# Optimization experiments

Measured on AMD Instinct MI355X. Metric: run time of the kernel, lower is better.

Reference implementation:

```python
import jax, jax.numpy as jnp
import numpy as np
from jax import lax

C = 64      # mid_channels
CR = 16     # reduced channels (C // reduction_ratio 4)
G = 4       # groups (C // group_channels 16)
K = 7       # involution kernel size
L = 6       # number of involution layers (n_layers - 2)
EPS = 1e-5
DN = ('NCHW', 'OIHW', 'NCHW')


def conv3(x, w, b):
    # 3x3 conv, stride 1, no padding (torch Conv2d default)
    y = lax.conv_general_dilated(x, w, (1, 1), [(0, 0), (0, 0)], dimension_numbers=DN)
    return y + b[None, :, None, None]


def conv1x1(x, w, b):
    # pointwise conv as einsum over channels
    return jnp.einsum('oi,bihw->bohw', w, x) + b[None, :, None, None]


def involution(x, wr, br, g, bt, mu, var, ws, bs):
    B, Cc, H, W = x.shape
    # kernel generation: 1x1 reduce -> BN (eval) -> ReLU -> 1x1 span
    t = conv1x1(x, wr, br)
    t = (t - mu[None, :, None, None]) * (g * jax.lax.rsqrt(var + EPS))[None, :, None, None] + bt[None, :, None, None]
    t = jax.nn.relu(t)
    w = conv1x1(t, ws, bs)                    # (B, G*K*K, H, W)
    w = w.reshape(B, G, K * K, H, W)
    # unfold: patches ordered (C, Kh, Kw) along channel dim, matching torch unfold
    p = lax.conv_general_dilated_patches(x, (K, K), (1, 1), [(K // 2, K // 2)] * 2, dimension_numbers=DN)
    p = p.reshape(B, G, Cc // G, K * K, H, W)
    out = jnp.einsum('bgkhw,bgckhw->bgchw', w, p)
    return out.reshape(B, Cc, H, W)


def setup_inputs() -> dict:
    key = jax.random.key(0)
    ks = jax.random.split(key, 9)
    s = 0.05
    return {
        'input_tensor': jax.random.normal(ks[0], (1, 3, 128, 128), jnp.float32),
        'conv_in_w': jax.random.normal(ks[1], (C, 3, 3, 3), jnp.float32) * s,
        'conv_in_b': jax.random.normal(ks[2], (C,), jnp.float32) * s,
        'w_reduce': jax.random.normal(ks[3], (L, CR, C), jnp.float32) * s,
        'b_reduce': jax.random.normal(ks[4], (L, CR), jnp.float32) * s,
        'bn_gamma': jnp.ones((L, CR), jnp.float32),
        'bn_beta': jnp.zeros((L, CR), jnp.float32),
        'bn_mean': jnp.zeros((L, CR), jnp.float32),
        'bn_var': jnp.ones((L, CR), jnp.float32),
        'w_span': jax.random.normal(ks[5], (L, G * K * K, CR), jnp.float32) * s,
        'b_span': jax.random.normal(ks[6], (L, G * K * K), jnp.float32) * s,
        'conv_out_w': jax.random.normal(ks[7], (2 * C, C, 3, 3), jnp.float32) * s,
        'conv_out_b': jax.random.normal(ks[8], (2 * C,), jnp.float32) * s,
    }


def reference(input_tensor, conv_in_w, conv_in_b, w_reduce, b_reduce, bn_gamma,
              bn_beta, bn_mean, bn_var, w_span, b_span, conv_out_w, conv_out_b):
    x = conv3(input_tensor, conv_in_w, conv_in_b)          # (1, 64, 126, 126)
    for i in range(L):
        x = jax.nn.relu(involution(x, w_reduce[i], b_reduce[i], bn_gamma[i],
                                   bn_beta[i], bn_mean[i], bn_var[i],
                                   w_span[i], b_span[i]))
    return conv3(x, conv_out_w, conv_out_b)                # (1, 128, 124, 124)
```

## Files before the change

### kernel.cpp

```cpp
#include <hip/hip_runtime.h>

#define IH 126
#define IW 126
#define HW 15876
#define OH 124
#define OW 124
#define OHW 15376

__global__ __launch_bounds__(256) void conv_in_kernel(
    const float* __restrict__ x, const float* __restrict__ w,
    const float* __restrict__ b, float* __restrict__ y)
{
  int pix = blockIdx.x * 256 + threadIdx.x;
  if (pix >= HW) return;
  int oc = blockIdx.y;
  int h  = pix / IW;
  int wc = pix - h * IW;
  const float* wp = w + oc * 27;
  float acc = b[oc];
#pragma unroll
  for (int ci = 0; ci < 3; ci++)
#pragma unroll
    for (int ky = 0; ky < 3; ky++)
#pragma unroll
      for (int kx = 0; kx < 3; kx++)
        acc = fmaf(x[ci * 128 * 128 + (h + ky) * 128 + (wc + kx)],
                   wp[ci * 9 + ky * 3 + kx], acc);
  y[oc * HW + pix] = acc;
}

__global__ __launch_bounds__(512, 4) void inv_kernel(
    const float* __restrict__ x, float* __restrict__ y,
    const float* __restrict__ wr, const float* __restrict__ br,
    const float* __restrict__ gam, const float* __restrict__ bet,
    const float* __restrict__ mu, const float* __restrict__ var,
    const float* __restrict__ wspan, const float* __restrict__ bspan)
{
  __shared__ __align__(16) char smem[63664];
  float* xs  = (float*)smem;
  float* wvs = (float*)(smem + 36400);
  float* tss = (float*)(smem + 61488);
  float* ob  = (float*)smem;

  int tid = threadIdx.x;
  int bx = blockIdx.x & 15, by = blockIdx.x >> 4;
  int ox0 = bx * 8, oy0 = by * 4;
  int xh0 = ox0 - 3, yh0 = oy0 - 3;

  for (int idx = tid; idx < 140 * 64; idx += 512) {
    int c = idx / 140;
    int pos = idx - c * 140;
    int row = pos / 14;
    int col = pos - row * 14;
    int gy = yh0 + row, gx = xh0 + col;
    float v = 0.f;
    if (gy >= 0 && gy < IH && gx >= 0 && gx < IW)
      v = x[c * HW + gy * IW + gx];
    xs[pos * 65 + c] = v;
  }
  __syncthreads();

  int w  = __builtin_amdgcn_readfirstlane(tid >> 6);
  int ln = tid & 63;
  int p  = ln & 31;
  int s  = ln >> 5;

  {
    int cr = 2 * w + s;
    int prow = p >> 3, pcol = p & 7;
    int pos = (prow + 3) * 14 + (pcol + 3);
    const float* xr = &xs[pos * 65];
    const float* wrr = wr + cr * 64;
    float a = 0.f;
#pragma unroll
    for (int c = 0; c < 64; c++) a = fmaf(xr[c], wrr[c], a);
    float sc = gam[cr] * rsqrtf(var[cr] + 1e-5f);
    float t = (a + br[cr] - mu[cr]) * sc + bet[cr];
    tss[p * 17 + cr] = fmaxf(t, 0.f);
  }
  __syncthreads();

  {
    int g  = w & 3;
    int q2 = (w >> 2) * 2 + s;
    float t16[16];
#pragma unroll
    for (int i = 0; i < 16; i++) t16[i] = tss[p * 17 + i];
    int prow = p >> 3, pcol = p & 7;
    const float* wsb = wspan + g * 49 * 16;
    const float* bsb = bspan + g * 49;
    for (int k = q2; k < 49; k += 4) {
      const float* wk = wsb + k * 16;
      float a = bsb[k];
#pragma unroll
      for (int i = 0; i < 16; i++) a = fmaf(t16[i], wk[i], a);
      wvs[((g * 49 + k) * 8 + pcol) * 4 + prow] = a;
    }
  }
  __syncthreads();

  float acc0 = 0.f, acc1 = 0.f, acc2 = 0.f, acc3 = 0.f;
  {
    int c = ln;
    int g = c >> 4;
    float xw[4][7];
#pragma unroll
    for (int r = 0; r < 4; r++)
#pragma unroll
      for (int kx = 0; kx < 7; kx++)
        xw[r][kx] = xs[(r * 14 + w + kx) * 65 + c];
#pragma unroll
    for (int ky = 0; ky < 7; ky++) {
      if (ky > 0) {
#pragma unroll
        for (int r = 0; r < 3; r++)
#pragma unroll
          for (int kx = 0; kx < 7; kx++) xw[r][kx] = xw[r + 1][kx];
#pragma unroll
        for (int kx = 0; kx < 7; kx++)
          xw[3][kx] = xs[((ky + 3) * 14 + w + kx) * 65 + c];
      }
#pragma unroll
      for (int kx = 0; kx < 7; kx++) {
        int k = ky * 7 + kx;
        float4 w4 = *(const float4*)&wvs[((g * 49 + k) * 8 + w) * 4];
        acc0 = fmaf(w4.x, xw[0][kx], acc0);
        acc1 = fmaf(w4.y, xw[1][kx], acc1);
        acc2 = fmaf(w4.z, xw[2][kx], acc2);
        acc3 = fmaf(w4.w, xw[3][kx], acc3);
      }
    }
  }
  __syncthreads();

  {
    int c = ln;
    ob[c * 33 + 0 * 8 + w] = fmaxf(acc0, 0.f);
    ob[c * 33 + 1 * 8 + w] = fmaxf(acc1, 0.f);
    ob[c * 33 + 2 * 8 + w] = fmaxf(acc2, 0.f);
    ob[c * 33 + 3 * 8 + w] = fmaxf(acc3, 0.f);
  }
  __syncthreads();
  for (int j = tid; j < 2048; j += 512) {
    int c = j >> 5, pp = j & 31;
    int prow = pp >> 3, pcol = pp & 7;
    int gy = oy0 + prow, gx = ox0 + pcol;
    if (gy < IH && gx < IW)
      y[c * HW + gy * IW + gx] = ob[c * 33 + pp];
  }
}

__global__ __launch_bounds__(256) void transpose_w_kernel(
    const float* __restrict__ w, float* __restrict__ wt)
{
  int i = blockIdx.x * 256 + threadIdx.x;
  if (i >= 128 * 64 * 9) return;
  int oc = i / 576;
  int rem = i - oc * 576;
  int ci = rem / 9;
  int k = rem - ci * 9;
  wt[(k * 64 + ci) * 128 + oc] = w[i];
}

__global__ __launch_bounds__(512, 4) void conv_out_kernel(
    const float* __restrict__ x, const float* __restrict__ wt,
    const float* __restrict__ b, float* __restrict__ y)
{
  __shared__ __align__(16) float xsm[16 * 100 * 4];
  int tid = threadIdx.x;
  int bx = blockIdx.x & 15, by = blockIdx.x >> 4;
  int oy0 = by * 8, ox0 = bx * 8;

  for (int u = tid; u < 1600; u += 512) {
    int cq = u / 100;
    int pos = u - cq * 100;
    int row = pos / 10;
    int col = pos - row * 10;
    int gy = oy0 + row, gx = ox0 + col;
    float4 v = make_float4(0.f, 0.f, 0.f, 0.f);
    if (gy < IH && gx < IW) {
      const float* xp = x + cq * 4 * HW + gy * IW + gx;
      v.x = xp[0]; v.y = xp[HW]; v.z = xp[2 * HW]; v.w = xp[3 * HW];
    }
    *(float4*)&xsm[u * 4] = v;
  }
  __syncthreads();

  int ln = tid & 63;
  int px = ln & 7, py = ln >> 3;
  int wv_ = __builtin_amdgcn_readfirstlane(tid >> 6);
  int oc8 = blockIdx.y * 64 + wv_ * 8;

  float acc[8];
#pragma unroll
  for (int j = 0; j < 8; j++) acc[j] = b[oc8 + j];

#pragma unroll
  for (int ky = 0; ky < 3; ky++) {
#pragma unroll
    for (int kx = 0; kx < 3; kx++) {
      int k = ky * 3 + kx;
      int pidx = (py + ky) * 10 + px + kx;
      const float* wp = wt + k * 64 * 128 + oc8;
#pragma unroll 4
      for (int cq = 0; cq < 16; cq++) {
        float4 xv = *(const float4*)&xsm[(cq * 100 + pidx) * 4];
        const float* wq = wp + cq * 4 * 128;
#pragma unroll
        for (int j = 0; j < 8; j++) {
          acc[j] = fmaf(xv.x, wq[0 * 128 + j], acc[j]);
          acc[j] = fmaf(xv.y, wq[1 * 128 + j], acc[j]);
          acc[j] = fmaf(xv.z, wq[2 * 128 + j], acc[j]);
          acc[j] = fmaf(xv.w, wq[3 * 128 + j], acc[j]);
        }
      }
    }
  }

  int oy = oy0 + py, ox = ox0 + px;
  if (oy < OH && ox < OW) {
#pragma unroll
    for (int j = 0; j < 8; j++)
      y[(oc8 + j) * OHW + oy * OW + ox] = acc[j];
  }
}

extern "C" void kernel_launch(void* const* d_in, const int* in_sizes, int n_in,
                              void* d_out, int out_size, void* d_ws, size_t ws_size,
                              hipStream_t stream)
{
  const float* input = (const float*)d_in[0];
  const float* ciw   = (const float*)d_in[1];
  const float* cib   = (const float*)d_in[2];
  const float* wred  = (const float*)d_in[3];
  const float* bred  = (const float*)d_in[4];
  const float* gam   = (const float*)d_in[5];
  const float* bet   = (const float*)d_in[6];
  const float* mu    = (const float*)d_in[7];
  const float* var   = (const float*)d_in[8];
  const float* wspan = (const float*)d_in[9];
  const float* bspan = (const float*)d_in[10];
  const float* cow   = (const float*)d_in[11];
  const float* cob   = (const float*)d_in[12];
  float* out = (float*)d_out;

  float* bufA = (float*)d_ws;
  float* bufB = bufA + (1 << 20);
  float* wt   = bufA + (1 << 21);

  transpose_w_kernel<<<288, 256, 0, stream>>>(cow, wt);
  conv_in_kernel<<<dim3(63, 64), 256, 0, stream>>>(input, ciw, cib, bufA);

  float* cur = bufA; float* nxt = bufB;
  for (int i = 0; i < 6; i++) {
    inv_kernel<<<512, 512, 0, stream>>>(cur, nxt,
        wred + i * 16 * 64, bred + i * 16, gam + i * 16, bet + i * 16,
        mu + i * 16, var + i * 16, wspan + i * 196 * 16, bspan + i * 196);
    float* t = cur; cur = nxt; nxt = t;
  }
  conv_out_kernel<<<dim3(256, 2), 512, 0, stream>>>(cur, wt, cob, out);
}
```

Baseline: 254.6 us.

## Vectorize involution kernel-gen LDS reads and split conv_out into smaller blocks

Pads the shared x tile to 68 floats per position so the 1x1 reduce can read channels as float4, and has each wave compute two reduced channels for all 64 lanes. The span step is redistributed so each wave handles every eighth (group,k) pair, and a 20-float padded stride for the reduced activations allows float4 loads. conv_out moves to 256-thread blocks covering 32 output channels across four grid rows, which gives more blocks and better occupancy. The costs are redundant compute in half-idle lanes, an extra barrier, and the x tile being loaded twice as often in conv_out.

Measured after the change: 253.2 us. Within noise of the previous version (-0.5%).

```diff
diff --git a/kernel.cpp b/kernel.cpp
--- a/kernel.cpp
+++ b/kernel.cpp
@@ -36,11 +36,10 @@
     const float* __restrict__ mu, const float* __restrict__ var,
     const float* __restrict__ wspan, const float* __restrict__ bspan)
 {
-  __shared__ __align__(16) char smem[63664];
-  float* xs  = (float*)smem;
-  float* wvs = (float*)(smem + 36400);
-  float* tss = (float*)(smem + 61488);
-  float* ob  = (float*)smem;
+  __shared__ __align__(16) float xs[140][68];
+  __shared__ __align__(16) float wvs[6272];
+  float* tss = &wvs[5632];
+  float* ob  = &xs[0][0];
 
   int tid = threadIdx.x;
   int bx = blockIdx.x & 15, by = blockIdx.x >> 4;
@@ -56,45 +55,58 @@
     float v = 0.f;
     if (gy >= 0 && gy < IH && gx >= 0 && gx < IW)
       v = x[c * HW + gy * IW + gx];
-    xs[pos * 65 + c] = v;
-  }
-  __syncthreads();
-
-  int w  = __builtin_amdgcn_readfirstlane(tid >> 6);
+    xs[pos][c] = v;
+  }
+  __syncthreads();
+
+  int w_ = __builtin_amdgcn_readfirstlane(tid >> 6);
   int ln = tid & 63;
   int p  = ln & 31;
-  int s  = ln >> 5;
-
-  {
-    int cr = 2 * w + s;
-    int prow = p >> 3, pcol = p & 7;
-    int pos = (prow + 3) * 14 + (pcol + 3);
-    const float* xr = &xs[pos * 65];
-    const float* wrr = wr + cr * 64;
-    float a = 0.f;
-#pragma unroll
-    for (int c = 0; c < 64; c++) a = fmaf(xr[c], wrr[c], a);
-    float sc = gam[cr] * rsqrtf(var[cr] + 1e-5f);
-    float t = (a + br[cr] - mu[cr]) * sc + bet[cr];
-    tss[p * 17 + cr] = fmaxf(t, 0.f);
-  }
-  __syncthreads();
-
-  {
-    int g  = w & 3;
-    int q2 = (w >> 2) * 2 + s;
-    float t16[16];
-#pragma unroll
-    for (int i = 0; i < 16; i++) t16[i] = tss[p * 17 + i];
-    int prow = p >> 3, pcol = p & 7;
-    const float* wsb = wspan + g * 49 * 16;
-    const float* bsb = bspan + g * 49;
-    for (int k = q2; k < 49; k += 4) {
-      const float* wk = wsb + k * 16;
-      float a = bsb[k];
-#pragma unroll
-      for (int i = 0; i < 16; i++) a = fmaf(t16[i], wk[i], a);
-      wvs[((g * 49 + k) * 8 + pcol) * 4 + prow] = a;
+  int prow = p >> 3, pcol = p & 7;
+  int pc = (prow + 3) * 14 + (pcol + 3);
+
+  {
+    int cr0 = 2 * w_;
+    const float* wa = wr + cr0 * 64;
+    const float* wb = wa + 64;
+    float a0 = 0.f, a1 = 0.f;
+#pragma unroll
+    for (int ci = 0; ci < 64; ci += 4) {
+      float4 xv = *(const float4*)&xs[pc][ci];
+      a0 = fmaf(xv.x, wa[ci + 0], a0); a1 = fmaf(xv.x, wb[ci + 0], a1);
+      a0 = fmaf(xv.y, wa[ci + 1], a0); a1 = fmaf(xv.y, wb[ci + 1], a1);
+      a0 = fmaf(xv.z, wa[ci + 2], a0); a1 = fmaf(xv.z, wb[ci + 2], a1);
+      a0 = fmaf(xv.w, wa[ci + 3], a0); a1 = fmaf(xv.w, wb[ci + 3], a1);
+    }
+    float s0 = gam[cr0]     * rsqrtf(var[cr0]     + 1e-5f);
+    float s1 = gam[cr0 + 1] * rsqrtf(var[cr0 + 1] + 1e-5f);
+    float t0 = (a0 + br[cr0]     - mu[cr0])     * s0 + bet[cr0];
+    float t1 = (a1 + br[cr0 + 1] - mu[cr0 + 1]) * s1 + bet[cr0 + 1];
+    if (ln < 32) {
+      tss[p * 20 + cr0]     = fmaxf(t0, 0.f);
+      tss[p * 20 + cr0 + 1] = fmaxf(t1, 0.f);
+    }
+  }
+  __syncthreads();
+
+  {
+    float tv[16];
+#pragma unroll
+    for (int i = 0; i < 4; i++) {
+      float4 t4 = *(const float4*)&tss[p * 20 + 4 * i];
+      tv[4 * i] = t4.x; tv[4 * i + 1] = t4.y;
+      tv[4 * i + 2] = t4.z; tv[4 * i + 3] = t4.w;
+    }
+    __syncthreads();
+    for (int j = 0; j < 25; j++) {
+      int pair = w_ + 8 * j;
+      if (pair < 196) {
+        const float* wk = wspan + pair * 16;
+        float a = bspan[pair];
+#pragma unroll
+        for (int i = 0; i < 16; i++) a = fmaf(tv[i], wk[i], a);
+        if (ln < 32) wvs[pair * 32 + pcol * 4 + prow] = a;
+      }
     }
   }
   __syncthreads();
@@ -102,13 +114,13 @@
   float acc0 = 0.f, acc1 = 0.f, acc2 = 0.f, acc3 = 0.f;
   {
     int c = ln;
-    int g = c >> 4;
+    int g = ln >> 4;
     float xw[4][7];
 #pragma unroll
     for (int r = 0; r < 4; r++)
 #pragma unroll
       for (int kx = 0; kx < 7; kx++)
-        xw[r][kx] = xs[(r * 14 + w + kx) * 65 + c];
+        xw[r][kx] = xs[r * 14 + w_ + kx][c];
 #pragma unroll
     for (int ky = 0; ky < 7; ky++) {
       if (ky > 0) {
@@ -118,12 +130,12 @@
           for (int kx = 0; kx < 7; kx++) xw[r][kx] = xw[r + 1][kx];
 #pragma unroll
         for (int kx = 0; kx < 7; kx++)
-          xw[3][kx] = xs[((ky + 3) * 14 + w + kx) * 65 + c];
+          xw[3][kx] = xs[(ky + 3) * 14 + w_ + kx][c];
       }
 #pragma unroll
       for (int kx = 0; kx < 7; kx++) {
         int k = ky * 7 + kx;
-        float4 w4 = *(const float4*)&wvs[((g * 49 + k) * 8 + w) * 4];
+        float4 w4 = *(const float4*)&wvs[(g * 49 + k) * 32 + w_ * 4];
         acc0 = fmaf(w4.x, xw[0][kx], acc0);
         acc1 = fmaf(w4.y, xw[1][kx], acc1);
         acc2 = fmaf(w4.z, xw[2][kx], acc2);
@@ -135,18 +147,18 @@
 
   {
     int c = ln;
-    ob[c * 33 + 0 * 8 + w] = fmaxf(acc0, 0.f);
-    ob[c * 33 + 1 * 8 + w] = fmaxf(acc1, 0.f);
-    ob[c * 33 + 2 * 8 + w] = fmaxf(acc2, 0.f);
-    ob[c * 33 + 3 * 8 + w] = fmaxf(acc3, 0.f);
+    ob[c * 33 + 0 * 8 + w_] = fmaxf(acc0, 0.f);
+    ob[c * 33 + 1 * 8 + w_] = fmaxf(acc1, 0.f);
+    ob[c * 33 + 2 * 8 + w_] = fmaxf(acc2, 0.f);
+    ob[c * 33 + 3 * 8 + w_] = fmaxf(acc3, 0.f);
   }
   __syncthreads();
   for (int j = tid; j < 2048; j += 512) {
-    int c = j >> 5, pp = j & 31;
-    int prow = pp >> 3, pcol = pp & 7;
-    int gy = oy0 + prow, gx = ox0 + pcol;
+    int c2 = j >> 5, pp = j & 31;
+    int pr = pp >> 3, pc2 = pp & 7;
+    int gy = oy0 + pr, gx = ox0 + pc2;
     if (gy < IH && gx < IW)
-      y[c * HW + gy * IW + gx] = ob[c * 33 + pp];
+      y[c2 * HW + gy * IW + gx] = ob[c2 * 33 + pp];
   }
 }
 
@@ -162,7 +174,7 @@
   wt[(k * 64 + ci) * 128 + oc] = w[i];
 }
 
-__global__ __launch_bounds__(512, 4) void conv_out_kernel(
+__global__ __launch_bounds__(256, 6) void conv_out_kernel(
     const float* __restrict__ x, const float* __restrict__ wt,
     const float* __restrict__ b, float* __restrict__ y)
 {
@@ -171,7 +183,7 @@
   int bx = blockIdx.x & 15, by = blockIdx.x >> 4;
   int oy0 = by * 8, ox0 = bx * 8;
 
-  for (int u = tid; u < 1600; u += 512) {
+  for (int u = tid; u < 1600; u += 256) {
     int cq = u / 100;
     int pos = u - cq * 100;
     int row = pos / 10;
@@ -189,7 +201,7 @@
   int ln = tid & 63;
   int px = ln & 7, py = ln >> 3;
   int wv_ = __builtin_amdgcn_readfirstlane(tid >> 6);
-  int oc8 = blockIdx.y * 64 + wv_ * 8;
+  int oc8 = blockIdx.y * 32 + wv_ * 8;
 
   float acc[8];
 #pragma unroll
@@ -258,5 +270,5 @@
         mu + i * 16, var + i * 16, wspan + i * 196 * 16, bspan + i * 196);
     float* t = cur; cur = nxt; nxt = t;
   }
-  conv_out_kernel<<<dim3(256, 2), 512, 0, stream>>>(cur, wt, cob, out);
-}
+  conv_out_kernel<<<dim3(256, 4), 256, 0, stream>>>(cur, wt, cob, out);
+}
```
